# Kernel optimization log

Measured on AMD Instinct MI355X. Metric: run time of the kernel, lower is better.

Reference implementation:

```python
import jax, jax.numpy as jnp
import numpy as np

N_ENT = 50000
N_REL = 237
DIM = 200
BATCH = 1024
N_EDGE_RAW = 400000
WALK_LEN = 3


def _build_graph():
    rng = np.random.default_rng(0)
    src = rng.integers(0, N_ENT, N_EDGE_RAW)
    dst = rng.integers(0, N_ENT, N_EDGE_RAW)
    key = np.unique(src.astype(np.int64) * N_ENT + dst.astype(np.int64))
    row = (key // N_ENT).astype(np.int64)
    col = (key % N_ENT).astype(np.int64)
    # symmetric D^{-1/2} A D^{-1/2} normalization (binary coalesced adjacency)
    deg = np.bincount(row, minlength=N_ENT).astype(np.float64)
    dinv = np.where(deg > 0, deg ** -0.5, 0.0)
    adj_val = (dinv[row] * dinv[col]).astype(np.float32)
    # random walk of length 3 from every node (torch_cluster.random_walk semantics)
    rowptr = np.concatenate([[0], np.cumsum(np.bincount(row, minlength=N_ENT))]).astype(np.int64)
    cur = np.arange(N_ENT)
    walk = [cur]
    for _ in range(WALK_LEN):
        d = rowptr[cur + 1] - rowptr[cur]
        off = np.floor(rng.random(N_ENT) * np.maximum(d, 1)).astype(np.int64)
        idx = np.minimum(rowptr[cur] + off, len(row) - 1)
        nxt = np.where(d > 0, col[idx], cur)
        walk.append(nxt)
        cur = nxt
    walk = np.stack(walk, 1)  # (N, WALK_LEN+1)
    # scatter(rw_adj, 1, walk, 1): binary rows, duplicates collapse; then D^{-1} row-normalize
    rw_key = np.unique(np.repeat(np.arange(N_ENT), WALK_LEN + 1).astype(np.int64) * N_ENT + walk.reshape(-1))
    rw_row = (rw_key // N_ENT).astype(np.int64)
    rw_col = (rw_key % N_ENT).astype(np.int64)
    rw_deg = np.bincount(rw_row, minlength=N_ENT).astype(np.float64)
    rw_val = (1.0 / np.maximum(rw_deg[rw_row], 1.0)).astype(np.float32)
    return row, col, adj_val, rw_row, rw_col, rw_val


def setup_inputs() -> dict:
    row, col, adj_val, rw_row, rw_col, rw_val = _build_graph()
    E = row.shape[0]
    key = jax.random.key(0)
    ks = jax.random.split(key, 12)
    g = 0.05
    return dict(
        entity_emb=jax.random.normal(ks[0], (N_ENT, DIM), jnp.float32) * g,
        rel_emb=jax.random.normal(ks[1], (2 * N_REL, DIM * DIM), jnp.float32) * 0.01,
        node_W1=jax.random.normal(ks[2], (2, DIM, DIM), jnp.float32) * g,
        node_b1=jnp.zeros((2, DIM), jnp.float32),
        node_W2=jax.random.normal(ks[3], (2, DIM, 1), jnp.float32) * g,
        node_b2=jnp.zeros((2, 1), jnp.float32),
        edge_W1=jax.random.normal(ks[4], (2, 2 * DIM, DIM), jnp.float32) * g,
        edge_b1=jnp.zeros((2, DIM), jnp.float32),
        edge_W2=jax.random.normal(ks[5], (2, DIM, 1), jnp.float32) * g,
        edge_b2=jnp.zeros((2, 1), jnp.float32),
        adj_row=jnp.asarray(row), adj_col=jnp.asarray(col), adj_val=jnp.asarray(adj_val),
        rw_row=jnp.asarray(rw_row), rw_col=jnp.asarray(rw_col), rw_val=jnp.asarray(rw_val),
        node_eps=jax.random.uniform(ks[6], (2, N_ENT, 1), jnp.float32),
        edge_eps=jax.random.uniform(ks[7], (2, E, 1), jnp.float32),
        sub=jax.random.randint(ks[8], (BATCH,), 0, N_ENT),
        rel=jax.random.randint(ks[9], (BATCH,), 0, 2 * N_REL),
        obj=jax.random.randint(ks[10], (BATCH,), 0, N_ENT),
        neg_tail=jax.random.randint(ks[11], (BATCH, 2), 0, N_ENT),
    )


def _spmm(row, col, val, x, n):
    # sparse COO (row, col, val) @ dense x, output (n, d)
    return jax.ops.segment_sum(val[:, None] * x[col], row, num_segments=n)


def _gate(logits, u):
    # concrete-gate noise: eps ~ U(bias, 1-bias); sigmoid((logit(eps)+logits)/0.5)
    bias = 1e-4
    eps = (2.0 * bias - 1.0) * u + (1.0 - bias)
    return jax.nn.sigmoid((jnp.log(eps) - jnp.log1p(-eps) + logits) / 0.5)


def reference(entity_emb, rel_emb, node_W1, node_b1, node_W2, node_b2,
              edge_W1, edge_b1, edge_W2, edge_b2,
              adj_row, adj_col, adj_val, rw_row, rw_col, rw_val,
              node_eps, edge_eps, sub, rel, obj, neg_tail):
    n, d = entity_emb.shape
    e0 = entity_emb
    node_masks, edge_masks = [], []
    edge_cat = jnp.concatenate([e0[adj_row], e0[adj_col]], axis=-1)  # (E, 2d)
    for i in range(2):
        h = jax.nn.relu(e0 @ node_W1[i] + node_b1[i])
        node_masks.append(_gate(h @ node_W2[i] + node_b2[i], node_eps[i]))  # (n,1)
        he = jax.nn.relu(edge_cat @ edge_W1[i] + edge_b1[i])
        edge_masks.append(_gate(he @ edge_W2[i] + edge_b2[i], edge_eps[i])[:, 0])  # (E,)
    # node-drop branch: mix self vs random-walk mean-pooled, then GCN propagate
    x_nd = e0
    for i in range(2):
        mp = _spmm(rw_row, rw_col, rw_val, x_nd, n)
        x_nd = node_masks[i] * x_nd + (1.0 - node_masks[i]) * mp
        x_nd = _spmm(adj_row, adj_col, adj_val, x_nd, n)
    # edge-drop branch: rw propagation twice; only the LAST edge mask is applied (as in source)
    x_ed = e0
    new_edge = adj_val
    for i in range(2):
        x_ed = _spmm(rw_row, rw_col, rw_val, x_ed, n)
        new_edge = adj_val * edge_masks[i]
    x_ed = _spmm(adj_row, adj_col, new_edge, x_ed, n)
    # RESCAL scoring against all entities
    lhs1 = e0[sub]                                   # (B, d)
    rel1 = rel_emb[rel].reshape(-1, d, d)            # (B, d, d)
    self_hr = jnp.einsum('bd,bde->be', lhs1, rel1)   # (B, d)
    scores = jax.nn.sigmoid(self_hr @ e0.T)          # (B, n)
    return scores, x_nd, x_ed
```

## Files before the change

### kernel.cpp

```cpp
#include <hip/hip_runtime.h>
#include <math.h>

#define DIMV 200
typedef unsigned short ushort;
typedef unsigned int uint;
typedef __attribute__((ext_vector_type(8))) __bf16  bf16x8;
typedef __attribute__((ext_vector_type(4))) float   f32x4;

static __device__ __forceinline__ int lower_bound(const int* __restrict__ a, int n, int key) {
    int lo = 0, hi = n;
    while (lo < hi) {
        int mid = (lo + hi) >> 1;
        if (a[mid] < key) lo = mid + 1; else hi = mid;
    }
    return lo;
}

static __device__ __forceinline__ float gate_fn(float u, float logit) {
    float ee = fmaf(u, -0.9998f, 0.9999f);
    float g  = (logf(ee) - log1pf(-ee) + logit) * 2.0f;
    return 1.0f / (1.0f + expf(-g));
}

static __device__ __forceinline__ ushort f2bf(float f) {
    unsigned int u = __float_as_uint(f);
    return (ushort)((u + 0x7fffu + ((u >> 16) & 1u)) >> 16);
}
static __device__ __forceinline__ float bf2f(ushort u) {
    return __uint_as_float(((unsigned int)u) << 16);
}
static __device__ __forceinline__ float2 bfp2f(uint u) {
    float2 r;
    r.x = __uint_as_float(u << 16);
    r.y = __uint_as_float(u & 0xffff0000u);
    return r;
}
static __device__ __forceinline__ uint f2bfp(float a, float b) {
    return (uint)f2bf(a) | ((uint)f2bf(b) << 16);
}

static __device__ __forceinline__ void cvt8_store(ushort* dst, const float* src) {
    float4 a = *(const float4*)src;
    float4 b = *(const float4*)(src + 4);
    dst[0] = f2bf(a.x); dst[1] = f2bf(a.y); dst[2] = f2bf(a.z); dst[3] = f2bf(a.w);
    dst[4] = f2bf(b.x); dst[5] = f2bf(b.y); dst[6] = f2bf(b.z); dst[7] = f2bf(b.w);
}
static __device__ __forceinline__ void zero8_store(ushort* dst) {
#pragma unroll
    for (int i = 0; i < 8; i++) dst[i] = 0;
}

__global__ __launch_bounds__(256) void e0bf_kernel(
    const float* __restrict__ e0, ushort* __restrict__ e0bf, int N)
{
    int idx = blockIdx.x * 256 + threadIdx.x;
    if (idx >= N * 28) return;
    int n = idx / 28, c = idx % 28;
    ushort* dst = e0bf + (size_t)n * 224 + c * 8;
    if (c < 25) cvt8_store(dst, e0 + (size_t)n * 200 + c * 8);
    else        zero8_store(dst);
}

__global__ __launch_bounds__(256) void transpose_w1e_kernel(
    const float* __restrict__ src, ushort* __restrict__ dst)
{
    int idx = blockIdx.x * 256 + threadIdx.x;
    if (idx >= 416 * 224) return;
    int n = idx / 224, k = idx % 224;
    float v = 0.f;
    if (k < 200) {
        if (n < 200)      v = src[k * 200 + n];
        else if (n < 400) v = src[(k + 200) * 200 + (n - 200)];
    }
    dst[idx] = f2bf(v);
}

__global__ __launch_bounds__(256) void transpose_w1n_kernel(
    const float* __restrict__ src, ushort* __restrict__ dst)
{
    int idx = blockIdx.x * 256 + threadIdx.x;
    int i = blockIdx.y;
    if (idx >= 208 * 224) return;
    int n = idx / 224, k = idx % 224;
    float v = (n < 200 && k < 200) ? src[i * 40000 + k * 200 + n] : 0.f;
    dst[(size_t)i * 208 * 224 + idx] = f2bf(v);
}

__global__ __launch_bounds__(256) void rowptr_kernel(
    const int* __restrict__ row, int E, int N, int* __restrict__ rowptr)
{
    int r = blockIdx.x * 256 + threadIdx.x;
    if (r <= N) rowptr[r] = lower_bound(row, E, r);
}

__global__ __launch_bounds__(256) void gemm_e0_kernel(
    const ushort* __restrict__ e0bf, const ushort* __restrict__ W1T,
    ushort* __restrict__ C, int M, int Cld, int Nvalid)
{
    __shared__ __align__(16) ushort As[2][128 * 40];
    __shared__ __align__(16) ushort Bs[2][208 * 40];

    const int t    = threadIdx.x;
    const int lane = t & 63;
    const int w    = t >> 6;
    const int q    = lane >> 4;
    const int ln   = lane & 15;
    const int r0   = blockIdx.x * 128;
    const int nb   = blockIdx.y;
    const ushort* Wt = W1T + (size_t)nb * 208 * 224;

    f32x4 acc[2][13];
#pragma unroll
    for (int mt = 0; mt < 2; mt++)
#pragma unroll
        for (int nt = 0; nt < 13; nt++) {
            acc[mt][nt][0] = 0.f; acc[mt][nt][1] = 0.f;
            acc[mt][nt][2] = 0.f; acc[mt][nt][3] = 0.f;
        }

    auto stageA = [&](int ks, int buf) {
#pragma unroll
        for (int it = 0; it < 2; it++) {
            int f = t + it * 256;
            int m = f >> 2, c4 = f & 3;
            int g = r0 + m;
            ushort* dst = &As[buf][m * 40 + c4 * 8];
            if (g < M) *(bf16x8*)dst = *(const bf16x8*)&e0bf[(size_t)g * 224 + ks * 32 + c4 * 8];
            else       zero8_store(dst);
        }
    };
    auto stageB = [&](int ks, int buf) {
        for (int f = t; f < 832; f += 256) {
            int n = f >> 2, c4 = f & 3;
            *(bf16x8*)&Bs[buf][n * 40 + c4 * 8] =
                *(const bf16x8*)&Wt[(size_t)n * 224 + ks * 32 + c4 * 8];
        }
    };

    stageA(0, 0); stageB(0, 0);
    __syncthreads();

    for (int ks = 0; ks < 7; ks++) {
        int cur = ks & 1;
        if (ks + 1 < 7) { stageA(ks + 1, cur ^ 1); stageB(ks + 1, cur ^ 1); }
        bf16x8 af0 = *(const bf16x8*)&As[cur][(w * 32 + ln) * 40 + q * 8];
        bf16x8 af1 = *(const bf16x8*)&As[cur][(w * 32 + 16 + ln) * 40 + q * 8];
#pragma unroll
        for (int nt = 0; nt < 13; nt++) {
            bf16x8 bf = *(const bf16x8*)&Bs[cur][(nt * 16 + ln) * 40 + q * 8];
            acc[0][nt] = __builtin_amdgcn_mfma_f32_16x16x32_bf16(af0, bf, acc[0][nt], 0, 0, 0);
            acc[1][nt] = __builtin_amdgcn_mfma_f32_16x16x32_bf16(af1, bf, acc[1][nt], 0, 0, 0);
        }
        __syncthreads();
    }

#pragma unroll
    for (int mt = 0; mt < 2; mt++) {
        int gm = r0 + w * 32 + mt * 16 + q * 4;
#pragma unroll
        for (int nt = 0; nt < 13; nt++) {
            int gn = nb * 208 + nt * 16 + ln;
            if (gn < Nvalid) {
#pragma unroll
                for (int r = 0; r < 4; r++)
                    if (gm + r < M) C[(size_t)(gm + r) * Cld + gn] = f2bf(acc[mt][nt][r]);
            }
        }
    }
}

__global__ __launch_bounds__(256) void edge_gate_kernel(
    const ushort* __restrict__ P, const float* __restrict__ b1,
    const float* __restrict__ W2, const float* __restrict__ b2,
    const float* __restrict__ eps, const int* __restrict__ erow,
    const int* __restrict__ ecol, float* __restrict__ mask_out, int E)
{
    const int lane = threadIdx.x & 63;
    const int wave = (blockIdx.x * 256 + threadIdx.x) >> 6;
    const int nw   = gridDim.x * 4;
    const int chunk = (E + nw - 1) / nw;
    const int e_lo = wave * chunk;
    const int e_hi = min(e_lo + chunk, E);

    float bb[4], ww[4];
#pragma unroll
    for (int j = 0; j < 4; j++) {
        int d = lane + j * 64;
        bool v = d < 200;
        bb[j] = v ? b1[d] : 0.f;
        ww[j] = v ? W2[d] : 0.f;
    }
    const float b2v = b2[0];

    for (int e = e_lo; e < e_hi; e++) {
        const ushort* pr = P + (size_t)erow[e] * 400;
        const ushort* pc = P + (size_t)ecol[e] * 400 + 200;
        float s = 0.f;
#pragma unroll
        for (int j = 0; j < 4; j++) {
            int d = lane + j * 64;
            if (d < 200)
                s = fmaf(fmaxf(bf2f(pr[d]) + bf2f(pc[d]) + bb[j], 0.f), ww[j], s);
        }
#pragma unroll
        for (int off = 32; off; off >>= 1) s += __shfl_xor(s, off);
        if (lane == 0) mask_out[e] = gate_fn(eps[e], s + b2v);
    }
}

__global__ __launch_bounds__(256) void node_mlp_mfma(
    const ushort* __restrict__ e0bf,
    const ushort* __restrict__ W1T,
    const float* __restrict__ b1, const float* __restrict__ W2,
    const float* __restrict__ b2, const float* __restrict__ eps,
    float* __restrict__ mask_out, int N)
{
    __shared__ __align__(16) ushort As[2][128 * 40];
    __shared__ __align__(16) ushort Bs[2][208 * 40];
    __shared__ float bsh[208], wsh[208];

    const int t    = threadIdx.x;
    const int lane = t & 63;
    const int w    = t >> 6;
    const int q    = lane >> 4;
    const int ln   = lane & 15;
    const int i    = blockIdx.y;
    const int r0   = blockIdx.x * 128;
    const ushort* Wt = W1T + (size_t)i * 208 * 224;

    if (t < 208) {
        bsh[t] = (t < 200) ? b1[i * 200 + t] : 0.f;
        wsh[t] = (t < 200) ? W2[i * 200 + t] : 0.f;
    }

    f32x4 acc[2][13];
#pragma unroll
    for (int mt = 0; mt < 2; mt++)
#pragma unroll
        for (int nt = 0; nt < 13; nt++) {
            acc[mt][nt][0] = 0.f; acc[mt][nt][1] = 0.f;
            acc[mt][nt][2] = 0.f; acc[mt][nt][3] = 0.f;
        }

    auto stageA = [&](int ks, int buf) {
#pragma unroll
        for (int it = 0; it < 2; it++) {
            int f = t + it * 256;
// ... 17 lines not shown

    for (int ks = 0; ks < 7; ks++) {
        int cur = ks & 1;
        if (ks + 1 < 7) { stageA(ks + 1, cur ^ 1); stageB(ks + 1, cur ^ 1); }
        bf16x8 af0 = *(const bf16x8*)&As[cur][(w * 32 + ln) * 40 + q * 8];
        bf16x8 af1 = *(const bf16x8*)&As[cur][(w * 32 + 16 + ln) * 40 + q * 8];
#pragma unroll
        for (int nt = 0; nt < 13; nt++) {
            bf16x8 bf = *(const bf16x8*)&Bs[cur][(nt * 16 + ln) * 40 + q * 8];
            acc[0][nt] = __builtin_amdgcn_mfma_f32_16x16x32_bf16(af0, bf, acc[0][nt], 0, 0, 0);
            acc[1][nt] = __builtin_amdgcn_mfma_f32_16x16x32_bf16(af1, bf, acc[1][nt], 0, 0, 0);
        }
        __syncthreads();
    }

    float p[2][4];
#pragma unroll
    for (int mt = 0; mt < 2; mt++)
#pragma unroll
        for (int r = 0; r < 4; r++) {
            float s = 0.f;
#pragma unroll
            for (int nt = 0; nt < 13; nt++) {
                int n = nt * 16 + ln;
                float h = fmaxf(acc[mt][nt][r] + bsh[n], 0.f);
                s = fmaf(h, wsh[n], s);
            }
            p[mt][r] = s;
        }
#pragma unroll
    for (int off = 1; off < 16; off <<= 1)
#pragma unroll
        for (int mt = 0; mt < 2; mt++)
#pragma unroll
            for (int r = 0; r < 4; r++)
                p[mt][r] += __shfl_xor(p[mt][r], off);

    if (ln == 0) {
        float b2v = b2[i];
        const float* epsi = eps + (size_t)i * N;
        float* outi = mask_out + (size_t)i * N;
#pragma unroll
        for (int mt = 0; mt < 2; mt++)
#pragma unroll
            for (int r = 0; r < 4; r++) {
                int g = r0 + w * 32 + mt * 16 + q * 4 + r;
                if (g < N) outi[g] = gate_fn(epsi[g], p[mt][r] + b2v);
            }
    }
}

__global__ __launch_bounds__(256) void scores_mfma(
    const ushort* __restrict__ hrbf, const ushort* __restrict__ e0bf,
    float* __restrict__ scores, int Nent)
{
    __shared__ __align__(16) ushort As[64 * 232];
    __shared__ __align__(16) ushort Bs[2][192 * 40];

    const int t    = threadIdx.x;
    const int lane = t & 63;
    const int w    = t >> 6;
    const int wm   = w >> 1, wn = w & 1;
    const int q    = lane >> 4;
    const int ln   = lane & 15;
    const int n0   = blockIdx.x * 192;
    const int b0   = blockIdx.y * 64;

    for (int f = t; f < 1792; f += 256) {
        int m = f / 28, c = f % 28;
        *(bf16x8*)&As[m * 232 + c * 8] = *(const bf16x8*)&hrbf[(size_t)(b0 + m) * 224 + c * 8];
    }

    auto stageB = [&](int ks, int buf) {
        for (int f = t; f < 768; f += 256) {
            int n = f >> 2, c4 = f & 3;
            int gn = n0 + n;
            ushort* dst = &Bs[buf][n * 40 + c4 * 8];
            if (gn < Nent) *(bf16x8*)dst = *(const bf16x8*)&e0bf[(size_t)gn * 224 + ks * 32 + c4 * 8];
            else           zero8_store(dst);
        }
    };
    stageB(0, 0);
    __syncthreads();

    f32x4 acc[2][6];
#pragma unroll
    for (int mt = 0; mt < 2; mt++)
#pragma unroll
        for (int nt = 0; nt < 6; nt++) {
            acc[mt][nt][0] = 0.f; acc[mt][nt][1] = 0.f;
            acc[mt][nt][2] = 0.f; acc[mt][nt][3] = 0.f;
        }

    for (int ks = 0; ks < 7; ks++) {
        int cur = ks & 1;
        if (ks + 1 < 7) stageB(ks + 1, cur ^ 1);
        bf16x8 af0 = *(const bf16x8*)&As[(wm * 32 + ln) * 232 + ks * 32 + q * 8];
        bf16x8 af1 = *(const bf16x8*)&As[(wm * 32 + 16 + ln) * 232 + ks * 32 + q * 8];
#pragma unroll
        for (int nt = 0; nt < 6; nt++) {
            bf16x8 bf = *(const bf16x8*)&Bs[cur][(wn * 96 + nt * 16 + ln) * 40 + q * 8];
            acc[0][nt] = __builtin_amdgcn_mfma_f32_16x16x32_bf16(af0, bf, acc[0][nt], 0, 0, 0);
            acc[1][nt] = __builtin_amdgcn_mfma_f32_16x16x32_bf16(af1, bf, acc[1][nt], 0, 0, 0);
        }
        __syncthreads();
    }

#pragma unroll
    for (int mt = 0; mt < 2; mt++) {
        int b = b0 + wm * 32 + mt * 16 + q * 4;
#pragma unroll
        for (int nt = 0; nt < 6; nt++) {
            int n = n0 + wn * 96 + nt * 16 + ln;
            if (n < Nent) {
#pragma unroll
                for (int r = 0; r < 4; r++)
                    scores[(size_t)(b + r) * Nent + n] = 1.f / (1.f + __expf(-acc[mt][nt][r]));
            }
        }
    }
}


__global__ __launch_bounds__(256) void spmm_bb(
    const uint* __restrict__ x, int xld, const int* __restrict__ rowptr,
    const int* __restrict__ col, const float* __restrict__ val,
    uint* __restrict__ out, int N)
{
    const int sub = threadIdx.x >> 7;
    const int d2  = threadIdx.x & 127;
    const int r   = blockIdx.x * 2 + sub;
    if (d2 >= 100 || r >= N) return;
    const int lo = rowptr[r], hi = rowptr[r + 1];
    float a0 = 0.f, a1 = 0.f, b0 = 0.f, b1 = 0.f;
    int e = lo;
    for (; e + 1 < hi; e += 2) {
        float2 xa = bfp2f(x[(size_t)col[e]     * xld + d2]);
        float2 xb = bfp2f(x[(size_t)col[e + 1] * xld + d2]);
        float v0 = val[e], v1 = val[e + 1];
        a0 = fmaf(v0, xa.x, a0); b0 = fmaf(v0, xa.y, b0);
        a1 = fmaf(v1, xb.x, a1); b1 = fmaf(v1, xb.y, b1);
    }
    if (e < hi) {
        float2 xa = bfp2f(x[(size_t)col[e] * xld + d2]);
        a0 = fmaf(val[e], xa.x, a0); b0 = fmaf(val[e], xa.y, b0);
    }
    out[(size_t)r * 100 + d2] = f2bfp(a0 + a1, b0 + b1);
}

__global__ __launch_bounds__(256) void rw_combine_bb(
    const uint* __restrict__ x, const int* __restrict__ rowptr,
    const int* __restrict__ col, const float* __restrict__ val,
    const float* __restrict__ mask, uint* __restrict__ out, int N)
{
    const int sub = threadIdx.x >> 7;
    const int d2  = threadIdx.x & 127;
    const int r   = blockIdx.x * 2 + sub;
    if (d2 >= 100 || r >= N) return;
    const int lo = rowptr[r], hi = rowptr[r + 1];
    float a0 = 0.f, a1 = 0.f, b0 = 0.f, b1 = 0.f;
    int e = lo;
    for (; e + 1 < hi; e += 2) {
        float2 xa = bfp2f(x[(size_t)col[e]     * 100 + d2]);
        float2 xb = bfp2f(x[(size_t)col[e + 1] * 100 + d2]);
        float v0 = val[e], v1 = val[e + 1];
        a0 = fmaf(v0, xa.x, a0); b0 = fmaf(v0, xa.y, b0);
        a1 = fmaf(v1, xb.x, a1); b1 = fmaf(v1, xb.y, b1);
    }
    if (e < hi) {
        float2 xa = bfp2f(x[(size_t)col[e] * 100 + d2]);
        a0 = fmaf(val[e], xa.x, a0); b0 = fmaf(val[e], xa.y, b0);
    }
    const float m = mask[r];
    float2 xs = bfp2f(x[(size_t)r * 100 + d2]);
    float sx = a0 + a1, sy = b0 + b1;
    out[(size_t)r * 100 + d2] = f2bfp(fmaf(m, xs.x - sx, sx), fmaf(m, xs.y - sy, sy));
}

__global__ __launch_bounds__(256) void spmm_dual_bb(
    const uint* __restrict__ xA, const uint* __restrict__ xB,
    const int* __restrict__ rowptr, const int* __restrict__ col,
    const float* __restrict__ val, const float* __restrict__ emask,
    float* __restrict__ outA, uint* __restrict__ outB, int N)
{
    const int sub = threadIdx.x >> 7;
    const int d2  = threadIdx.x & 127;
    const int r   = blockIdx.x * 2 + sub;
    if (d2 >= 100 || r >= N) return;
    const int lo = rowptr[r], hi = rowptr[r + 1];
    float a0 = 0.f, a1 = 0.f, b0 = 0.f, b1 = 0.f;
    float c0 = 0.f, c1 = 0.f, d0 = 0.f, d1 = 0.f;
// ... 11 lines not shown
        c1 = fmaf(v1, xb1.x, c1);  d1 = fmaf(v1, xb1.y, d1);
    }
    if (e < hi) {
        size_t o0 = (size_t)col[e] * 100 + d2;
        float v0 = val[e], vm0 = v0 * emask[e];
        float2 xa0 = bfp2f(xA[o0]);
        float2 xb0 = bfp2f(xB[o0]);
        a0 = fmaf(vm0, xa0.x, a0); b0 = fmaf(vm0, xa0.y, b0);
        c0 = fmaf(v0, xb0.x, c0);  d0 = fmaf(v0, xb0.y, d0);
    }
    float2 oA; oA.x = a0 + a1; oA.y = b0 + b1;
    ((float2*)outA)[(size_t)r * 100 + d2] = oA;
    outB[(size_t)r * 100 + d2] = f2bfp(c0 + c1, d0 + d1);
}

__global__ __launch_bounds__(256) void spmm_bf32(
    const uint* __restrict__ x, const int* __restrict__ rowptr,
    const int* __restrict__ col, const float* __restrict__ val,
    float* __restrict__ out, int N)
{
    const int sub = threadIdx.x >> 7;
    const int d2  = threadIdx.x & 127;
    const int r   = blockIdx.x * 2 + sub;
    if (d2 >= 100 || r >= N) return;
    const int lo = rowptr[r], hi = rowptr[r + 1];
    float a0 = 0.f, a1 = 0.f, b0 = 0.f, b1 = 0.f;
    int e = lo;
    for (; e + 1 < hi; e += 2) {
        float2 xa = bfp2f(x[(size_t)col[e]     * 100 + d2]);
        float2 xb = bfp2f(x[(size_t)col[e + 1] * 100 + d2]);
        float v0 = val[e], v1 = val[e + 1];
        a0 = fmaf(v0, xa.x, a0); b0 = fmaf(v0, xa.y, b0);
        a1 = fmaf(v1, xb.x, a1); b1 = fmaf(v1, xb.y, b1);
    }
    if (e < hi) {
        float2 xa = bfp2f(x[(size_t)col[e] * 100 + d2]);
        a0 = fmaf(val[e], xa.x, a0); b0 = fmaf(val[e], xa.y, b0);
    }
    float2 o; o.x = a0 + a1; o.y = b0 + b1;
    ((float2*)out)[(size_t)r * 100 + d2] = o;
}

__global__ __launch_bounds__(256) void combine_bb(
    const float* __restrict__ e0, const uint* __restrict__ mp,
    const float* __restrict__ mask, uint* __restrict__ out, int N)
{
    int idx = blockIdx.x * 256 + threadIdx.x;
    if (idx >= N * 100) return;
    float m = mask[idx / 100];
    float2 a = ((const float2*)e0)[idx];
    float2 b = bfp2f(mp[idx]);
    out[idx] = f2bfp(fmaf(m, a.x - b.x, b.x), fmaf(m, a.y - b.y, b.y));
}

__global__ __launch_bounds__(256) void selfhr_kernel(
    const float* __restrict__ e0, const float* __restrict__ rel_emb,
    const int* __restrict__ sub, const int* __restrict__ rel,
    ushort* __restrict__ hrbf)
{
    const int b = blockIdx.x;
    __shared__ float lhs[DIMV];
    const int t = threadIdx.x;
    if (t < DIMV) lhs[t] = e0[(size_t)sub[b] * DIMV + t];
    __syncthreads();
    if (t >= 224) return;
    if (t < DIMV) {
        const float* R = rel_emb + (size_t)rel[b] * (DIMV * DIMV);
        float acc = 0.f;
        for (int dd = 0; dd < DIMV; dd++)
            acc = fmaf(lhs[dd], R[dd * DIMV + t], acc);
        hrbf[(size_t)b * 224 + t] = f2bf(acc);
    } else {
        hrbf[(size_t)b * 224 + t] = 0;
    }
}

extern "C" void kernel_launch(void* const* d_in, const int* in_sizes, int n_in,
                              void* d_out, int out_size, void* d_ws, size_t ws_size,
                              hipStream_t stream)
{
    const float* e0       = (const float*)d_in[0];
    const float* rel_emb  = (const float*)d_in[1];
    const float* node_W1  = (const float*)d_in[2];
    const float* node_b1  = (const float*)d_in[3];
    const float* node_W2  = (const float*)d_in[4];
    const float* node_b2  = (const float*)d_in[5];
    const float* edge_W1  = (const float*)d_in[6];
    const float* edge_b1  = (const float*)d_in[7];
// ... 21 lines not shown
    ushort* hrbf = e0bf + (size_t)N * 224;
    float*  fb   = (float*)(hrbf + (size_t)B * 224);
    float*  node_mask = fb;
    float*  edge_mask = node_mask + 2 * (size_t)N;
    int*    rp_adj = (int*)(edge_mask + E);
    int*    rp_rw  = rp_adj + (N + 1);

    float* out    = (float*)d_out;
    float* scores = out;
    float* x_nd   = out + (size_t)B * N;
    float* x_ed   = x_nd + (size_t)N * DIMV;
    uint*   Tb   = (uint*)scores;
    uint*   T2b  = Tb   + (size_t)N * 100;
    uint*   xndb = T2b  + (size_t)N * 100;
    uint*   Tnb  = xndb + (size_t)N * 100;
    ushort* Pb   = (ushort*)(Tnb + (size_t)N * 100);

    const int grid2 = (N + 1) / 2;

    e0bf_kernel<<<(N * 28 + 255) / 256, 256, 0, stream>>>(e0, e0bf, N);
    transpose_w1e_kernel<<<(416 * 224 + 255) / 256, 256, 0, stream>>>(edge_W1 + 400 * 200, W1eT);
    transpose_w1n_kernel<<<dim3((208 * 224 + 255) / 256, 2), 256, 0, stream>>>(node_W1, W1nT);
    rowptr_kernel<<<(N + 256) / 256, 256, 0, stream>>>(adj_row, E,   N, rp_adj);
    rowptr_kernel<<<(N + 256) / 256, 256, 0, stream>>>(rw_row,  Erw, N, rp_rw);

    gemm_e0_kernel<<<dim3((N + 127) / 128, 2), 256, 0, stream>>>(e0bf, W1eT, Pb, N, 400, 400);
    edge_gate_kernel<<<6144, 256, 0, stream>>>(
        Pb, edge_b1 + 200, edge_W2 + 200, edge_b2 + 1, edge_eps + (size_t)E,
        adj_row, adj_col, edge_mask, E);

    node_mlp_mfma<<<dim3((N + 127) / 128, 2), 256, 0, stream>>>(
        e0bf, W1nT, node_b1, node_W2, node_b2, node_eps, node_mask, N);

    spmm_bb<<<grid2, 256, 0, stream>>>((const uint*)e0bf, 112, rp_rw, rw_col, rw_val, Tb, N);

    spmm_bb<<<grid2, 256, 0, stream>>>(Tb, 100, rp_rw, rw_col, rw_val, T2b, N);

    combine_bb<<<(N * 100 + 255) / 256, 256, 0, stream>>>(e0, Tb, node_mask, xndb, N);

    spmm_dual_bb<<<grid2, 256, 0, stream>>>(T2b, xndb, rp_adj, adj_col, adj_val,
                                            edge_mask, x_ed, Tnb, N);

    rw_combine_bb<<<grid2, 256, 0, stream>>>(Tnb, rp_rw, rw_col, rw_val, node_mask + N, T2b, N);
    spmm_bf32<<<grid2, 256, 0, stream>>>(T2b, rp_adj, adj_col, adj_val, x_nd, N);

    selfhr_kernel<<<B, 256, 0, stream>>>(e0, rel_emb, sub, rel, hrbf);

    scores_mfma<<<dim3((N + 191) / 192, B / 64), 256, 0, stream>>>(hrbf, e0bf, scores, N);
}
```

Measured before the change: 978.1 us.

## Merge prep kernels, fuse edge/node MLP GEMMs, and co-schedule SpMM with gates

Folds the bf16 conversion, weight transposes, rowptr searches and self_hr computation into one multi-role prep kernel. The edge-projection GEMM and node MLP are merged into a single launch with a swizzled block order. The first random-walk SpMM is co-launched with the edge gate, and the second with the combine step. The scores GEMM now uses 128-row batch tiles with A fragments read straight from global memory and a grouped block order. The aim is to cut launch count, improve L2 locality and overlap independent work, at the cost of heavier branching per block and higher register pressure in the scores kernel.

After: 936.6 us. -4.2%, faster.

```diff
diff --git a/kernel.cpp b/kernel.cpp
--- a/kernel.cpp
+++ b/kernel.cpp
@@ -26,9 +26,6 @@
     unsigned int u = __float_as_uint(f);
     return (ushort)((u + 0x7fffu + ((u >> 16) & 1u)) >> 16);
 }
-static __device__ __forceinline__ float bf2f(ushort u) {
-    return __uint_as_float(((unsigned int)u) << 16);
-}
 static __device__ __forceinline__ float2 bfp2f(uint u) {
     float2 r;
     r.x = __uint_as_float(u << 16);
@@ -50,187 +47,118 @@
     for (int i = 0; i < 8; i++) dst[i] = 0;
 }
 
-__global__ __launch_bounds__(256) void e0bf_kernel(
-    const float* __restrict__ e0, ushort* __restrict__ e0bf, int N)
-{
-    int idx = blockIdx.x * 256 + threadIdx.x;
-    if (idx >= N * 28) return;
-    int n = idx / 28, c = idx % 28;
-    ushort* dst = e0bf + (size_t)n * 224 + c * 8;
-    if (c < 25) cvt8_store(dst, e0 + (size_t)n * 200 + c * 8);
-    else        zero8_store(dst);
-}
-
-__global__ __launch_bounds__(256) void transpose_w1e_kernel(
-    const float* __restrict__ src, ushort* __restrict__ dst)
-{
-    int idx = blockIdx.x * 256 + threadIdx.x;
-    if (idx >= 416 * 224) return;
-    int n = idx / 224, k = idx % 224;
-    float v = 0.f;
-    if (k < 200) {
-        if (n < 200)      v = src[k * 200 + n];
-        else if (n < 400) v = src[(k + 200) * 200 + (n - 200)];
-    }
-    dst[idx] = f2bf(v);
-}
-
-__global__ __launch_bounds__(256) void transpose_w1n_kernel(
-    const float* __restrict__ src, ushort* __restrict__ dst)
-{
-    int idx = blockIdx.x * 256 + threadIdx.x;
-    int i = blockIdx.y;
-    if (idx >= 208 * 224) return;
-    int n = idx / 224, k = idx % 224;
-    float v = (n < 200 && k < 200) ? src[i * 40000 + k * 200 + n] : 0.f;
-    dst[(size_t)i * 208 * 224 + idx] = f2bf(v);
-}
-
-__global__ __launch_bounds__(256) void rowptr_kernel(
-    const int* __restrict__ row, int E, int N, int* __restrict__ rowptr)
-{
-    int r = blockIdx.x * 256 + threadIdx.x;
-    if (r <= N) rowptr[r] = lower_bound(row, E, r);
-}
-
-__global__ __launch_bounds__(256) void gemm_e0_kernel(
-    const ushort* __restrict__ e0bf, const ushort* __restrict__ W1T,
-    ushort* __restrict__ C, int M, int Cld, int Nvalid)
+__global__ __launch_bounds__(256) void prep_all(
+    const float* __restrict__ e0, ushort* __restrict__ e0bf,
+    const float* __restrict__ w1e_src, ushort* __restrict__ W1eT,
+    const float* __restrict__ w1n_src, ushort* __restrict__ W1nT,
+    const int* __restrict__ adj_row, int E, int* __restrict__ rp_adj,
+    const int* __restrict__ rw_row, int Erw, int* __restrict__ rp_rw,
+    const float* __restrict__ rel_emb, const int* __restrict__ sub,
+    const int* __restrict__ rel, ushort* __restrict__ hrbf, int N)
+{
+    __shared__ float lhs[DIMV];
+    int bid = blockIdx.x;
+    const int t = threadIdx.x;
+
+    const int NB0 = (N * 28 + 255) >> 8;
+    if (bid < NB0) {
+        int idx = bid * 256 + t;
+        if (idx < N * 28) {
+            int n = idx / 28, c = idx % 28;
+            ushort* dst = e0bf + (size_t)n * 224 + c * 8;
+            if (c < 25) cvt8_store(dst, e0 + (size_t)n * 200 + c * 8);
+            else        zero8_store(dst);
+        }
+        return;
+    }
+    bid -= NB0;
+    if (bid < 364) {
+        int idx = bid * 256 + t;
+        if (idx < 416 * 224) {
+            int n = idx / 224, k = idx % 224;
+            float v = 0.f;
+            if (k < 200) {
+                if (n < 200)      v = w1e_src[k * 200 + n];
+                else if (n < 400) v = w1e_src[(k + 200) * 200 + (n - 200)];
+            }
+            W1eT[idx] = f2bf(v);
+        }
+        return;
+    }
+    bid -= 364;
+    if (bid < 364) {
+        int i = bid / 182;
+        int idx = (bid % 182) * 256 + t;
+        if (idx < 208 * 224) {
+            int n = idx / 224, k = idx % 224;
+            float v = (n < 200 && k < 200) ? w1n_src[i * 40000 + k * 200 + n] : 0.f;
+            W1nT[(size_t)i * 208 * 224 + idx] = f2bf(v);
+        }
+        return;
+    }
+    bid -= 364;
+    const int NBr = (N + 256) >> 8;
+    if (bid < NBr) {
+        int r = bid * 256 + t;
+        if (r <= N) rp_adj[r] = lower_bound(adj_row, E, r);
+        return;
+    }
+    bid -= NBr;
+    if (bid < NBr) {
+        int r = bid * 256 + t;
+        if (r <= N) rp_rw[r] = lower_bound(rw_row, Erw, r);
+        return;
+    }
+    bid -= NBr;
+    {
+        const int b = bid;
+        if (t < DIMV) lhs[t] = e0[(size_t)sub[b] * DIMV + t];
+        __syncthreads();
+        if (t >= 224) return;
+        if (t < DIMV) {
+            const float* R = rel_emb + (size_t)rel[b] * (DIMV * DIMV);
+            float acc = 0.f;
+            for (int dd = 0; dd < DIMV; dd++)
+                acc = fmaf(lhs[dd], R[dd * DIMV + t], acc);
+            hrbf[(size_t)b * 224 + t] = f2bf(acc);
+        } else {
+            hrbf[(size_t)b * 224 + t] = 0;
+        }
+    }
+}
+
+__global__ __launch_bounds__(256) void fused_mlp(
+    const ushort* __restrict__ e0bf, const ushort* __restrict__ W1eT,
+    const ushort* __restrict__ W1nT, ushort* __restrict__ Pb,
+    const float* __restrict__ nb1, const float* __restrict__ nW2,
+    const float* __restrict__ nb2, const float* __restrict__ neps,
+    float* __restrict__ node_mask, int N, int GX)
 {
     __shared__ __align__(16) ushort As[2][128 * 40];
     __shared__ __align__(16) ushort Bs[2][208 * 40];
+    __shared__ float bsh[208], wsh[208];
+
+    const int r8  = blockIdx.x & 7;
+    const int rem = blockIdx.x >> 3;
+    const int y   = rem & 3;
+    const int q4  = rem >> 2;
+    const int x   = r8 + 8 * q4;
+    if (x >= GX) return;
 
     const int t    = threadIdx.x;
     const int lane = t & 63;
     const int w    = t >> 6;
     const int q    = lane >> 4;
     const int ln   = lane & 15;
-    const int r0   = blockIdx.x * 128;
-    const int nb   = blockIdx.y;
-    const ushort* Wt = W1T + (size_t)nb * 208 * 224;
-
-    f32x4 acc[2][13];
-#pragma unroll
-    for (int mt = 0; mt < 2; mt++)
-#pragma unroll
-        for (int nt = 0; nt < 13; nt++) {
-            acc[mt][nt][0] = 0.f; acc[mt][nt][1] = 0.f;
-            acc[mt][nt][2] = 0.f; acc[mt][nt][3] = 0.f;
-        }
-
-    auto stageA = [&](int ks, int buf) {
-#pragma unroll
-        for (int it = 0; it < 2; it++) {
-            int f = t + it * 256;
-            int m = f >> 2, c4 = f & 3;
-            int g = r0 + m;
-            ushort* dst = &As[buf][m * 40 + c4 * 8];
-            if (g < M) *(bf16x8*)dst = *(const bf16x8*)&e0bf[(size_t)g * 224 + ks * 32 + c4 * 8];
-            else       zero8_store(dst);
-        }
-    };
-    auto stageB = [&](int ks, int buf) {
-        for (int f = t; f < 832; f += 256) {
-            int n = f >> 2, c4 = f & 3;
-            *(bf16x8*)&Bs[buf][n * 40 + c4 * 8] =
-                *(const bf16x8*)&Wt[(size_t)n * 224 + ks * 32 + c4 * 8];
-        }
-    };
-
-    stageA(0, 0); stageB(0, 0);
-    __syncthreads();
-
-    for (int ks = 0; ks < 7; ks++) {
-        int cur = ks & 1;
-        if (ks + 1 < 7) { stageA(ks + 1, cur ^ 1); stageB(ks + 1, cur ^ 1); }
-        bf16x8 af0 = *(const bf16x8*)&As[cur][(w * 32 + ln) * 40 + q * 8];
-        bf16x8 af1 = *(const bf16x8*)&As[cur][(w * 32 + 16 + ln) * 40 + q * 8];
-#pragma unroll
-        for (int nt = 0; nt < 13; nt++) {
-            bf16x8 bf = *(const bf16x8*)&Bs[cur][(nt * 16 + ln) * 40 + q * 8];
-            acc[0][nt] = __builtin_amdgcn_mfma_f32_16x16x32_bf16(af0, bf, acc[0][nt], 0, 0, 0);
-            acc[1][nt] = __builtin_amdgcn_mfma_f32_16x16x32_bf16(af1, bf, acc[1][nt], 0, 0, 0);
-        }
-        __syncthreads();
-    }
-
-#pragma unroll
-    for (int mt = 0; mt < 2; mt++) {
-        int gm = r0 + w * 32 + mt * 16 + q * 4;
-#pragma unroll
-        for (int nt = 0; nt < 13; nt++) {
-            int gn = nb * 208 + nt * 16 + ln;
-            if (gn < Nvalid) {
-#pragma unroll
-                for (int r = 0; r < 4; r++)
-                    if (gm + r < M) C[(size_t)(gm + r) * Cld + gn] = f2bf(acc[mt][nt][r]);
-            }
-        }
-    }
-}
-
-__global__ __launch_bounds__(256) void edge_gate_kernel(
-    const ushort* __restrict__ P, const float* __restrict__ b1,
-    const float* __restrict__ W2, const float* __restrict__ b2,
-    const float* __restrict__ eps, const int* __restrict__ erow,
-    const int* __restrict__ ecol, float* __restrict__ mask_out, int E)
-{
-    const int lane = threadIdx.x & 63;
-    const int wave = (blockIdx.x * 256 + threadIdx.x) >> 6;
-    const int nw   = gridDim.x * 4;
-    const int chunk = (E + nw - 1) / nw;
-    const int e_lo = wave * chunk;
-    const int e_hi = min(e_lo + chunk, E);
-
-    float bb[4], ww[4];
-#pragma unroll
-    for (int j = 0; j < 4; j++) {
-        int d = lane + j * 64;
-        bool v = d < 200;
-        bb[j] = v ? b1[d] : 0.f;
-        ww[j] = v ? W2[d] : 0.f;
-    }
-    const float b2v = b2[0];
-
-    for (int e = e_lo; e < e_hi; e++) {
-        const ushort* pr = P + (size_t)erow[e] * 400;
-        const ushort* pc = P + (size_t)ecol[e] * 400 + 200;
-        float s = 0.f;
-#pragma unroll
-        for (int j = 0; j < 4; j++) {
-            int d = lane + j * 64;
-            if (d < 200)
-                s = fmaf(fmaxf(bf2f(pr[d]) + bf2f(pc[d]) + bb[j], 0.f), ww[j], s);
-        }
-#pragma unroll
-        for (int off = 32; off; off >>= 1) s += __shfl_xor(s, off);
-        if (lane == 0) mask_out[e] = gate_fn(eps[e], s + b2v);
-    }
-}
-
-__global__ __launch_bounds__(256) void node_mlp_mfma(
-    const ushort* __restrict__ e0bf,
-    const ushort* __restrict__ W1T,
-    const float* __restrict__ b1, const float* __restrict__ W2,
-    const float* __restrict__ b2, const float* __restrict__ eps,
-    float* __restrict__ mask_out, int N)
-{
-    __shared__ __align__(16) ushort As[2][128 * 40];
-    __shared__ __align__(16) ushort Bs[2][208 * 40];
-    __shared__ float bsh[208], wsh[208];
-
-    const int t    = threadIdx.x;
-    const int lane = t & 63;
-    const int w    = t >> 6;
-    const int q    = lane >> 4;
-    const int ln   = lane & 15;
-    const int i    = blockIdx.y;
-    const int r0   = blockIdx.x * 128;
-    const ushort* Wt = W1T + (size_t)i * 208 * 224;
-
-    if (t < 208) {
-        bsh[t] = (t < 200) ? b1[i * 200 + t] : 0.f;
-        wsh[t] = (t < 200) ? W2[i * 200 + t] : 0.f;
+    const int r0   = x * 128;
+    const bool edge = (y < 2);
+    const int  i    = y - 2;
+    const ushort* Wt = edge ? (W1eT + (size_t)y * 208 * 224)
+                            : (W1nT + (size_t)i * 208 * 224);
+
+    if (!edge && t < 208) {
+        bsh[t] = (t < 200) ? nb1[i * 200 + t] : 0.f;
+        wsh[t] = (t < 200) ? nW2[i * 200 + t] : 0.f;
     }
 
     f32x4 acc[2][13];
@@ -278,122 +206,66 @@
         __syncthreads();
     }
 
-    float p[2][4];
-#pragma unroll
-    for (int mt = 0; mt < 2; mt++)
-#pragma unroll
-        for (int r = 0; r < 4; r++) {
-            float s = 0.f;
+    if (edge) {
+#pragma unroll
+        for (int mt = 0; mt < 2; mt++) {
+            int gm = r0 + w * 32 + mt * 16 + q * 4;
 #pragma unroll
             for (int nt = 0; nt < 13; nt++) {
-                int n = nt * 16 + ln;
-                float h = fmaxf(acc[mt][nt][r] + bsh[n], 0.f);
-                s = fmaf(h, wsh[n], s);
+                int gn = y * 208 + nt * 16 + ln;
+                if (gn < 400) {
+#pragma unroll
+                    for (int r = 0; r < 4; r++)
+                        if (gm + r < N) Pb[(size_t)(gm + r) * 400 + gn] = f2bf(acc[mt][nt][r]);
+                }
             }
-            p[mt][r] = s;
-        }
-#pragma unroll
-    for (int off = 1; off < 16; off <<= 1)
+        }
+    } else {
+        float p[2][4];
 #pragma unroll
         for (int mt = 0; mt < 2; mt++)
 #pragma unroll
-            for (int r = 0; r < 4; r++)
-                p[mt][r] += __shfl_xor(p[mt][r], off);
-
-    if (ln == 0) {
-        float b2v = b2[i];
-        const float* epsi = eps + (size_t)i * N;
-        float* outi = mask_out + (size_t)i * N;
-#pragma unroll
-        for (int mt = 0; mt < 2; mt++)
-#pragma unroll
             for (int r = 0; r < 4; r++) {
-                int g = r0 + w * 32 + mt * 16 + q * 4 + r;
-                if (g < N) outi[g] = gate_fn(epsi[g], p[mt][r] + b2v);
+                float s = 0.f;
+#pragma unroll
+                for (int nt = 0; nt < 13; nt++) {
+                    int n = nt * 16 + ln;
+                    float h = fmaxf(acc[mt][nt][r] + bsh[n], 0.f);
+                    s = fmaf(h, wsh[n], s);
+                }
+                p[mt][r] = s;
             }
-    }
-}
-
-__global__ __launch_bounds__(256) void scores_mfma(
-    const ushort* __restrict__ hrbf, const ushort* __restrict__ e0bf,
-    float* __restrict__ scores, int Nent)
-{
-    __shared__ __align__(16) ushort As[64 * 232];
-    __shared__ __align__(16) ushort Bs[2][192 * 40];
-
-    const int t    = threadIdx.x;
-    const int lane = t & 63;
-    const int w    = t >> 6;
-    const int wm   = w >> 1, wn = w & 1;
-    const int q    = lane >> 4;
-    const int ln   = lane & 15;
-    const int n0   = blockIdx.x * 192;
-    const int b0   = blockIdx.y * 64;
-
-    for (int f = t; f < 1792; f += 256) {
-        int m = f / 28, c = f % 28;
-        *(bf16x8*)&As[m * 232 + c * 8] = *(const bf16x8*)&hrbf[(size_t)(b0 + m) * 224 + c * 8];
-    }
-
-    auto stageB = [&](int ks, int buf) {
-        for (int f = t; f < 768; f += 256) {
-            int n = f >> 2, c4 = f & 3;
-            int gn = n0 + n;
-            ushort* dst = &Bs[buf][n * 40 + c4 * 8];
-            if (gn < Nent) *(bf16x8*)dst = *(const bf16x8*)&e0bf[(size_t)gn * 224 + ks * 32 + c4 * 8];
-            else           zero8_store(dst);
-        }
-    };
-    stageB(0, 0);
-    __syncthreads();
-
-    f32x4 acc[2][6];
-#pragma unroll
-    for (int mt = 0; mt < 2; mt++)
-#pragma unroll
-        for (int nt = 0; nt < 6; nt++) {
-            acc[mt][nt][0] = 0.f; acc[mt][nt][1] = 0.f;
-            acc[mt][nt][2] = 0.f; acc[mt][nt][3] = 0.f;
-        }
-
-    for (int ks = 0; ks < 7; ks++) {
-        int cur = ks & 1;
-        if (ks + 1 < 7) stageB(ks + 1, cur ^ 1);
-        bf16x8 af0 = *(const bf16x8*)&As[(wm * 32 + ln) * 232 + ks * 32 + q * 8];
-        bf16x8 af1 = *(const bf16x8*)&As[(wm * 32 + 16 + ln) * 232 + ks * 32 + q * 8];
-#pragma unroll
-        for (int nt = 0; nt < 6; nt++) {
-            bf16x8 bf = *(const bf16x8*)&Bs[cur][(wn * 96 + nt * 16 + ln) * 40 + q * 8];
-            acc[0][nt] = __builtin_amdgcn_mfma_f32_16x16x32_bf16(af0, bf, acc[0][nt], 0, 0, 0);
-            acc[1][nt] = __builtin_amdgcn_mfma_f32_16x16x32_bf16(af1, bf, acc[1][nt], 0, 0, 0);
-        }
-        __syncthreads();
-    }
-
-#pragma unroll
-    for (int mt = 0; mt < 2; mt++) {
-        int b = b0 + wm * 32 + mt * 16 + q * 4;
-#pragma unroll
-        for (int nt = 0; nt < 6; nt++) {
-            int n = n0 + wn * 96 + nt * 16 + ln;
-            if (n < Nent) {
+#pragma unroll
+        for (int off = 1; off < 16; off <<= 1)
+#pragma unroll
+            for (int mt = 0; mt < 2; mt++)
 #pragma unroll
                 for (int r = 0; r < 4; r++)
-                    scores[(size_t)(b + r) * Nent + n] = 1.f / (1.f + __expf(-acc[mt][nt][r]));
-            }
-        }
-    }
-}
-
-
-__global__ __launch_bounds__(256) void spmm_bb(
+                    p[mt][r] += __shfl_xor(p[mt][r], off);
+
+        if (ln == 0) {
+            float b2v = nb2[i];
+            const float* epsi = neps + (size_t)i * N;
+            float* outi = node_mask + (size_t)i * N;
+#pragma unroll
+            for (int mt = 0; mt < 2; mt++)
+#pragma unroll
+                for (int r = 0; r < 4; r++) {
+                    int g = r0 + w * 32 + mt * 16 + q * 4 + r;
+                    if (g < N) outi[g] = gate_fn(epsi[g], p[mt][r] + b2v);
+                }
+        }
+    }
+}
+
+static __device__ __forceinline__ void spmm_bb_body(
     const uint* __restrict__ x, int xld, const int* __restrict__ rowptr,
     const int* __restrict__ col, const float* __restrict__ val,
-    uint* __restrict__ out, int N)
-{
-    const int sub = threadIdx.x >> 7;
-    const int d2  = threadIdx.x & 127;
-    const int r   = blockIdx.x * 2 + sub;
+    uint* __restrict__ out, int N, int bid, int t)
+{
+    const int sub = t >> 7;
+    const int d2  = t & 127;
+    const int r   = bid * 2 + sub;
     if (d2 >= 100 || r >= N) return;
     const int lo = rowptr[r], hi = rowptr[r + 1];
     float a0 = 0.f, a1 = 0.f, b0 = 0.f, b1 = 0.f;
@@ -412,33 +284,100 @@
     out[(size_t)r * 100 + d2] = f2bfp(a0 + a1, b0 + b1);
 }
 
-__global__ __launch_bounds__(256) void rw_combine_bb(
-    const uint* __restrict__ x, const int* __restrict__ rowptr,
-    const int* __restrict__ col, const float* __restrict__ val,
-    const float* __restrict__ mask, uint* __restrict__ out, int N)
-{
-    const int sub = threadIdx.x >> 7;
-    const int d2  = threadIdx.x & 127;
-    const int r   = blockIdx.x * 2 + sub;
-    if (d2 >= 100 || r >= N) return;
-    const int lo = rowptr[r], hi = rowptr[r + 1];
-    float a0 = 0.f, a1 = 0.f, b0 = 0.f, b1 = 0.f;
-    int e = lo;
-    for (; e + 1 < hi; e += 2) {
-        float2 xa = bfp2f(x[(size_t)col[e]     * 100 + d2]);
-        float2 xb = bfp2f(x[(size_t)col[e + 1] * 100 + d2]);
-        float v0 = val[e], v1 = val[e + 1];
-        a0 = fmaf(v0, xa.x, a0); b0 = fmaf(v0, xa.y, b0);
-        a1 = fmaf(v1, xb.x, a1); b1 = fmaf(v1, xb.y, b1);
-    }
-    if (e < hi) {
-        float2 xa = bfp2f(x[(size_t)col[e] * 100 + d2]);
-        a0 = fmaf(val[e], xa.x, a0); b0 = fmaf(val[e], xa.y, b0);
-    }
-    const float m = mask[r];
-    float2 xs = bfp2f(x[(size_t)r * 100 + d2]);
-    float sx = a0 + a1, sy = b0 + b1;
-    out[(size_t)r * 100 + d2] = f2bfp(fmaf(m, xs.x - sx, sx), fmaf(m, xs.y - sy, sy));
+__global__ __launch_bounds__(256) void k3_rw1_egate(
+    const uint* __restrict__ e0u, const int* __restrict__ rp_rw,
+    const int* __restrict__ rw_col, const float* __restrict__ rw_val,
+    uint* __restrict__ Tb,
+    const uint* __restrict__ P4, const int* __restrict__ rp_adj,
+    const int* __restrict__ adj_col,
+    const float* __restrict__ b1, const float* __restrict__ W2,
+    const float* __restrict__ b2, const float* __restrict__ eps,
+    float* __restrict__ edge_mask, int N, int NB_SP)
+{
+    int bid = blockIdx.x;
+    const int t = threadIdx.x;
+    if (bid < NB_SP) {
+        spmm_bb_body(e0u, 112, rp_rw, rw_col, rw_val, Tb, N, bid, t);
+        return;
+    }
+    bid -= NB_SP;
+    const int lane = t & 63;
+    const int w    = t >> 6;
+    const int gw   = bid * 4 + w;
+    const bool act1 = lane < 36;
+    const int dA = 2 * lane;
+    const int dB = 128 + 2 * lane;
+    const float bb0x = b1[dA], bb0y = b1[dA + 1];
+    const float ww0x = W2[dA], ww0y = W2[dA + 1];
+    const float bb1x = act1 ? b1[dB] : 0.f, bb1y = act1 ? b1[dB + 1] : 0.f;
+    const float ww1x = act1 ? W2[dB] : 0.f, ww1y = act1 ? W2[dB + 1] : 0.f;
+    const float b2v = b2[0];
+
+    const int r_lo = gw * 2;
+    const int r_hi = min(r_lo + 2, N);
+    for (int r = r_lo; r < r_hi; r++) {
+        const uint* Pr = P4 + (size_t)r * 200;
+        float2 a0 = bfp2f(Pr[lane]);
+        float2 a1; a1.x = 0.f; a1.y = 0.f;
+        if (act1) a1 = bfp2f(Pr[64 + lane]);
+        a0.x += bb0x; a0.y += bb0y; a1.x += bb1x; a1.y += bb1y;
+        const int lo = rp_adj[r], hi = rp_adj[r + 1];
+        int e = lo;
+        for (; e + 1 < hi; e += 2) {
+            const uint* Pc0 = P4 + (size_t)adj_col[e]     * 200 + 100;
+            const uint* Pc1 = P4 + (size_t)adj_col[e + 1] * 200 + 100;
+            float2 q00 = bfp2f(Pc0[lane]);
+            float2 q10 = bfp2f(Pc1[lane]);
+            float2 q01, q11; q01.x = q01.y = q11.x = q11.y = 0.f;
+            if (act1) { q01 = bfp2f(Pc0[64 + lane]); q11 = bfp2f(Pc1[64 + lane]); }
+            float s0 = fmaxf(a0.x + q00.x, 0.f) * ww0x + fmaxf(a0.y + q00.y, 0.f) * ww0y
+                     + fmaxf(a1.x + q01.x, 0.f) * ww1x + fmaxf(a1.y + q01.y, 0.f) * ww1y;
+            float s1 = fmaxf(a0.x + q10.x, 0.f) * ww0x + fmaxf(a0.y + q10.y, 0.f) * ww0y
+                     + fmaxf(a1.x + q11.x, 0.f) * ww1x + fmaxf(a1.y + q11.y, 0.f) * ww1y;
+#pragma unroll
+            for (int off = 32; off; off >>= 1) {
+                s0 += __shfl_xor(s0, off);
+                s1 += __shfl_xor(s1, off);
+            }
+            if (lane == 0) {
+                edge_mask[e]     = gate_fn(eps[e],     s0 + b2v);
+                edge_mask[e + 1] = gate_fn(eps[e + 1], s1 + b2v);
+            }
+        }
+        if (e < hi) {
+            const uint* Pc0 = P4 + (size_t)adj_col[e] * 200 + 100;
+            float2 q00 = bfp2f(Pc0[lane]);
+            float2 q01; q01.x = q01.y = 0.f;
+            if (act1) q01 = bfp2f(Pc0[64 + lane]);
+            float s0 = fmaxf(a0.x + q00.x, 0.f) * ww0x + fmaxf(a0.y + q00.y, 0.f) * ww0y
+                     + fmaxf(a1.x + q01.x, 0.f) * ww1x + fmaxf(a1.y + q01.y, 0.f) * ww1y;
+#pragma unroll
+            for (int off = 32; off; off >>= 1) s0 += __shfl_xor(s0, off);
+            if (lane == 0) edge_mask[e] = gate_fn(eps[e], s0 + b2v);
+        }
+    }
+}
+
+__global__ __launch_bounds__(256) void k4_rw2_combine(
+    const uint* __restrict__ Tb, const int* __restrict__ rp_rw,
+    const int* __restrict__ rw_col, const float* __restrict__ rw_val,
+    uint* __restrict__ T2b,
+    const float* __restrict__ e0, const float* __restrict__ mask,
+    uint* __restrict__ xndb, int N, int NB_SP)
+{
+    int bid = blockIdx.x;
+    const int t = threadIdx.x;
+    if (bid < NB_SP) {
+        spmm_bb_body(Tb, 100, rp_rw, rw_col, rw_val, T2b, N, bid, t);
+        return;
+    }
+    bid -= NB_SP;
+    int idx = bid * 256 + t;
+    if (idx >= N * 100) return;
+    float m = mask[idx / 100];
+    float2 a = ((const float2*)e0)[idx];
+    float2 b = bfp2f(Tb[idx]);
+    xndb[idx] = f2bfp(fmaf(m, a.x - b.x, b.x), fmaf(m, a.y - b.y, b.y));
 }
 
 __global__ __launch_bounds__(256) void spmm_dual_bb(
@@ -480,10 +419,10 @@
     outB[(size_t)r * 100 + d2] = f2bfp(c0 + c1, d0 + d1);
 }
 
-__global__ __launch_bounds__(256) void spmm_bf32(
+__global__ __launch_bounds__(256) void rw_combine_bb(
     const uint* __restrict__ x, const int* __restrict__ rowptr,
     const int* __restrict__ col, const float* __restrict__ val,
-    float* __restrict__ out, int N)
+    const float* __restrict__ mask, uint* __restrict__ out, int N)
 {
     const int sub = threadIdx.x >> 7;
     const int d2  = threadIdx.x & 127;
@@ -503,41 +442,115 @@
         float2 xa = bfp2f(x[(size_t)col[e] * 100 + d2]);
         a0 = fmaf(val[e], xa.x, a0); b0 = fmaf(val[e], xa.y, b0);
     }
+    const float m = mask[r];
+    float2 xs = bfp2f(x[(size_t)r * 100 + d2]);
+    float sx = a0 + a1, sy = b0 + b1;
+    out[(size_t)r * 100 + d2] = f2bfp(fmaf(m, xs.x - sx, sx), fmaf(m, xs.y - sy, sy));
+}
+
+__global__ __launch_bounds__(256) void spmm_bf32(
+    const uint* __restrict__ x, const int* __restrict__ rowptr,
+    const int* __restrict__ col, const float* __restrict__ val,
+    float* __restrict__ out, int N)
+{
+    const int sub = threadIdx.x >> 7;
+    const int d2  = threadIdx.x & 127;
+    const int r   = blockIdx.x * 2 + sub;
+    if (d2 >= 100 || r >= N) return;
+    const int lo = rowptr[r], hi = rowptr[r + 1];
+    float a0 = 0.f, a1 = 0.f, b0 = 0.f, b1 = 0.f;
+    int e = lo;
+    for (; e + 1 < hi; e += 2) {
+        float2 xa = bfp2f(x[(size_t)col[e]     * 100 + d2]);
+        float2 xb = bfp2f(x[(size_t)col[e + 1] * 100 + d2]);
+        float v0 = val[e], v1 = val[e + 1];
+        a0 = fmaf(v0, xa.x, a0); b0 = fmaf(v0, xa.y, b0);
+        a1 = fmaf(v1, xb.x, a1); b1 = fmaf(v1, xb.y, b1);
+    }
+    if (e < hi) {
+        float2 xa = bfp2f(x[(size_t)col[e] * 100 + d2]);
+        a0 = fmaf(val[e], xa.x, a0); b0 = fmaf(val[e], xa.y, b0);
+    }
     float2 o; o.x = a0 + a1; o.y = b0 + b1;
     ((float2*)out)[(size_t)r * 100 + d2] = o;
 }
 
-__global__ __launch_bounds__(256) void combine_bb(
-    const float* __restrict__ e0, const uint* __restrict__ mp,
-    const float* __restrict__ mask, uint* __restrict__ out, int N)
-{
-    int idx = blockIdx.x * 256 + threadIdx.x;
-    if (idx >= N * 100) return;
-    float m = mask[idx / 100];
-    float2 a = ((const float2*)e0)[idx];
-    float2 b = bfp2f(mp[idx]);
-    out[idx] = f2bfp(fmaf(m, a.x - b.x, b.x), fmaf(m, a.y - b.y, b.y));
-}
-
-__global__ __launch_bounds__(256) void selfhr_kernel(
-    const float* __restrict__ e0, const float* __restrict__ rel_emb,
-    const int* __restrict__ sub, const int* __restrict__ rel,
-    ushort* __restrict__ hrbf)
-{
-    const int b = blockIdx.x;
-    __shared__ float lhs[DIMV];
-    const int t = threadIdx.x;
-    if (t < DIMV) lhs[t] = e0[(size_t)sub[b] * DIMV + t];
+__global__ __launch_bounds__(256) void scores_mfma(
+    const ushort* __restrict__ hrbf, const ushort* __restrict__ e0bf,
+    float* __restrict__ scores, int Nent, int GX)
+{
+    __shared__ __align__(16) ushort Bs[2][192 * 40];
+
+    const int r8  = blockIdx.x & 7;
+    const int rem = blockIdx.x >> 3;
+    const int y   = rem & 7;
+    const int q8  = rem >> 3;
+    const int x   = r8 + 8 * q8;
+    if (x >= GX) return;
+
+    const int t    = threadIdx.x;
+    const int lane = t & 63;
+    const int w    = t >> 6;
+    const int q    = lane >> 4;
+    const int ln   = lane & 15;
+    const int n0   = x * 192;
+    const int b0   = y * 128;
+    const int arow = b0 + w * 32 + ln;
+
+    auto stageB = [&](int ks, int buf) {
+        for (int f = t; f < 768; f += 256) {
+            int n = f >> 2, c4 = f & 3;
+            int gn = n0 + n;
+            ushort* dst = &Bs[buf][n * 40 + c4 * 8];
+            if (gn < Nent) *(bf16x8*)dst = *(const bf16x8*)&e0bf[(size_t)gn * 224 + ks * 32 + c4 * 8];
+            else           zero8_store(dst);
+        }
+    };
+    stageB(0, 0);
+
+    f32x4 acc[2][12];
+#pragma unroll
+    for (int mt = 0; mt < 2; mt++)
+#pragma unroll
+        for (int nt = 0; nt < 12; nt++) {
+            acc[mt][nt][0] = 0.f; acc[mt][nt][1] = 0.f;
+            acc[mt][nt][2] = 0.f; acc[mt][nt][3] = 0.f;
+        }
+
+    bf16x8 a0 = *(const bf16x8*)&hrbf[(size_t)arow * 224 + q * 8];
+    bf16x8 a1 = *(const bf16x8*)&hrbf[(size_t)(arow + 16) * 224 + q * 8];
     __syncthreads();
-    if (t >= 224) return;
-    if (t < DIMV) {
-        const float* R = rel_emb + (size_t)rel[b] * (DIMV * DIMV);
-        float acc = 0.f;
-        for (int dd = 0; dd < DIMV; dd++)
-            acc = fmaf(lhs[dd], R[dd * DIMV + t], acc);
-        hrbf[(size_t)b * 224 + t] = f2bf(acc);
-    } else {
-        hrbf[(size_t)b * 224 + t] = 0;
+
+    for (int ks = 0; ks < 7; ks++) {
+        int cur = ks & 1;
+        bf16x8 a0n = a0, a1n = a1;
+        if (ks + 1 < 7) {
+            stageB(ks + 1, cur ^ 1);
+            a0n = *(const bf16x8*)&hrbf[(size_t)arow * 224 + (ks + 1) * 32 + q * 8];
+            a1n = *(const bf16x8*)&hrbf[(size_t)(arow + 16) * 224 + (ks + 1) * 32 + q * 8];
+        }
+#pragma unroll
+        for (int nt = 0; nt < 12; nt++) {
+            bf16x8 bf = *(const bf16x8*)&Bs[cur][(nt * 16 + ln) * 40 + q * 8];
+            acc[0][nt] = __builtin_amdgcn_mfma_f32_16x16x32_bf16(a0, bf, acc[0][nt], 0, 0, 0);
+            acc[1][nt] = __builtin_amdgcn_mfma_f32_16x16x32_bf16(a1, bf, acc[1][nt], 0, 0, 0);
+        }
+        __syncthreads();
+        a0 = a0n; a1 = a1n;
+    }
+
+#pragma unroll
+    for (int mt = 0; mt < 2; mt++) {
+        int b = b0 + w * 32 + mt * 16 + q * 4;
+#pragma unroll
+        for (int nt = 0; nt < 12; nt++) {
+            int n = n0 + nt * 16 + ln;
+            if (n < Nent) {
+#pragma unroll
+                for (int r = 0; r < 4; r++)
+                    scores[(size_t)(b + r) * Nent + n] = 1.f / (1.f + __expf(-acc[mt][nt][r]));
+            }
+        }
     }
 }
 
@@ -589,37 +602,41 @@
     uint*   T2b  = Tb   + (size_t)N * 100;
     uint*   xndb = T2b  + (size_t)N * 100;
     uint*   Tnb  = xndb + (size_t)N * 100;
-    ushort* Pb   = (ushort*)(Tnb + (size_t)N * 100);
-
-    const int grid2 = (N + 1) / 2;
-
-    e0bf_kernel<<<(N * 28 + 255) / 256, 256, 0, stream>>>(e0, e0bf, N);
-    transpose_w1e_kernel<<<(416 * 224 + 255) / 256, 256, 0, stream>>>(edge_W1 + 400 * 200, W1eT);
-    transpose_w1n_kernel<<<dim3((208 * 224 + 255) / 256, 2), 256, 0, stream>>>(node_W1, W1nT);
-    rowptr_kernel<<<(N + 256) / 256, 256, 0, stream>>>(adj_row, E,   N, rp_adj);
-    rowptr_kernel<<<(N + 256) / 256, 256, 0, stream>>>(rw_row,  Erw, N, rp_rw);
-
-    gemm_e0_kernel<<<dim3((N + 127) / 128, 2), 256, 0, stream>>>(e0bf, W1eT, Pb, N, 400, 400);
-    edge_gate_kernel<<<6144, 256, 0, stream>>>(
-        Pb, edge_b1 + 200, edge_W2 + 200, edge_b2 + 1, edge_eps + (size_t)E,
-        adj_row, adj_col, edge_mask, E);
-
-    node_mlp_mfma<<<dim3((N + 127) / 128, 2), 256, 0, stream>>>(
-        e0bf, W1nT, node_b1, node_W2, node_b2, node_eps, node_mask, N);
-
-    spmm_bb<<<grid2, 256, 0, stream>>>((const uint*)e0bf, 112, rp_rw, rw_col, rw_val, Tb, N);
-
-    spmm_bb<<<grid2, 256, 0, stream>>>(Tb, 100, rp_rw, rw_col, rw_val, T2b, N);
-
-    combine_bb<<<(N * 100 + 255) / 256, 256, 0, stream>>>(e0, Tb, node_mask, xndb, N);
-
-    spmm_dual_bb<<<grid2, 256, 0, stream>>>(T2b, xndb, rp_adj, adj_col, adj_val,
-                                            edge_mask, x_ed, Tnb, N);
-
-    rw_combine_bb<<<grid2, 256, 0, stream>>>(Tnb, rp_rw, rw_col, rw_val, node_mask + N, T2b, N);
-    spmm_bf32<<<grid2, 256, 0, stream>>>(T2b, rp_adj, adj_col, adj_val, x_nd, N);
-
-    selfhr_kernel<<<B, 256, 0, stream>>>(e0, rel_emb, sub, rel, hrbf);
-
-    scores_mfma<<<dim3((N + 191) / 192, B / 64), 256, 0, stream>>>(hrbf, e0bf, scores, N);
-}
+    uint*   Pb   = Tnb  + (size_t)N * 100;
+
+    const int NB_SP = (N + 1) / 2;
+    const int NB0   = (N * 28 + 255) / 256;
+    const int NBr   = (N + 256) / 256;
+    const int prep_blocks = NB0 + 364 + 364 + NBr + NBr + B;
+    const int GXg = (N + 127) / 128;
+    const int GXs = (N + 191) / 192;
+
+    prep_all<<<prep_blocks, 256, 0, stream>>>(
+        e0, e0bf, edge_W1 + 400 * 200, W1eT, node_W1, W1nT,
+        adj_row, E, rp_adj, rw_row, Erw, rp_rw,
+        rel_emb, sub, rel, hrbf, N);
+
+    fused_mlp<<<32 * ((GXg + 7) / 8), 256, 0, stream>>>(
+        e0bf, W1eT, W1nT, (ushort*)Pb,
+        node_b1, node_W2, node_b2, node_eps, node_mask, N, GXg);
+
+    k3_rw1_egate<<<NB_SP + (NB_SP + 3) / 4, 256, 0, stream>>>(
+        (const uint*)e0bf, rp_rw, rw_col, rw_val, Tb,
+        Pb, rp_adj, adj_col,
+        edge_b1 + 200, edge_W2 + 200, edge_b2 + 1, edge_eps + (size_t)E,
+        edge_mask, N, NB_SP);
+
+    k4_rw2_combine<<<NB_SP + (N * 100 + 255) / 256, 256, 0, stream>>>(
+        Tb, rp_rw, rw_col, rw_val, T2b, e0, node_mask, xndb, N, NB_SP);
+
+    spmm_dual_bb<<<NB_SP, 256, 0, stream>>>(
+        T2b, xndb, rp_adj, adj_col, adj_val, edge_mask, x_ed, Tnb, N);
+
+    rw_combine_bb<<<NB_SP, 256, 0, stream>>>(
+        Tnb, rp_rw, rw_col, rw_val, node_mask + N, T2b, N);
+
+    spmm_bf32<<<NB_SP, 256, 0, stream>>>(T2b, rp_adj, adj_col, adj_val, x_nd, N);
+
+    scores_mfma<<<64 * ((GXs + 7) / 8), 256, 0, stream>>>(
+        hrbf, e0bf, scores, N, GXs);
+}
```
